# Optimization experiments

Hardware: AMD Instinct MI355X
Metric: run time of the kernel (lower is better)

## Reference

```python
import jax, jax.numpy as jnp
import numpy as np

N = 200000   # nodes
R = 4        # relations
E = 1000000  # edges per relation
B = 1024     # graphs in batch


def _graph_conv(h, s, d, ew, W, b):
    """DGL GraphConv, norm='both', optional edge_weight. h:[N,F_in] -> [N,F_out]."""
    n = h.shape[0]
    ones = jnp.ones(s.shape[0], dtype=h.dtype)
    out_deg = jnp.clip(jax.ops.segment_sum(ones, s, num_segments=n), 1.0)
    in_deg = jnp.clip(jax.ops.segment_sum(ones, d, num_segments=n), 1.0)
    hs = h * jax.lax.rsqrt(out_deg)[:, None]          # src-side norm
    m = hs[s]                                         # gather: [E, F_in]
    if ew is not None:
        m = m * ew[:, None]
    agg = jax.ops.segment_sum(m, d, num_segments=n)   # scatter-sum: [N, F_in]
    rst = agg * jax.lax.rsqrt(in_deg)[:, None]        # dst-side norm
    return rst @ W + b


def _hetero_layer(h, src, dst, ew, W, b):
    out = None
    for r in range(R):
        ewr = None if ew is None else ew[r]
        o = _graph_conv(h, src[r], dst[r], ewr, W[r], b[r])
        out = o if out is None else out + o
    return out


def setup_inputs() -> dict:
    key = jax.random.key(0)
    ks = jax.random.split(key, 10)
    feat = jax.random.normal(ks[0], (N, 2), dtype=jnp.float32)
    src = jax.random.randint(ks[1], (R, E), 0, N, dtype=jnp.int32)
    dst = jax.random.randint(ks[2], (R, E), 0, N, dtype=jnp.int32)
    ew = jax.random.uniform(ks[3], (R, E), dtype=jnp.float32)
    graph_ids = jnp.sort(jax.random.randint(ks[4], (N,), 0, B, dtype=jnp.int32))
    W1 = jax.random.normal(ks[5], (R, 2, 16), dtype=jnp.float32) * 0.5
    b1 = jnp.zeros((R, 16), dtype=jnp.float32)
    W2 = jax.random.normal(ks[6], (R, 16, 16), dtype=jnp.float32) * 0.25
    b2 = jnp.zeros((R, 16), dtype=jnp.float32)
    Wc = jax.random.normal(ks[7], (16, 2), dtype=jnp.float32) * 0.25
    bc = jnp.zeros((2,), dtype=jnp.float32)
    return {"feat": feat, "src": src, "dst": dst, "ew": ew,
            "graph_ids": graph_ids, "W1": W1, "b1": b1,
            "W2": W2, "b2": b2, "Wc": Wc, "bc": bc}


def reference(feat, src, dst, ew, graph_ids, W1, b1, W2, b2, Wc, bc):
    # layer 1: per-relation weighted GraphConv, summed over relations
    h = _hetero_layer(feat, src, dst, ew, W1, b1)
    h = jax.nn.relu(h)
    # layer 2: no edge weights (kwargs not forwarded in original code)
    h = _hetero_layer(h, src, dst, None, W2, b2)
    # mean_nodes per graph in the batch
    sums = jax.ops.segment_sum(h, graph_ids, num_segments=B)          # [B,16]
    cnts = jax.ops.segment_sum(jnp.ones((N,), h.dtype), graph_ids, num_segments=B)
    hg = sums / jnp.clip(cnts, 1.0)[:, None]
    return hg @ Wc + bc                                               # [B,2]
```

## Files before the change

kernel.cpp:

```cpp
#include <hip/hip_runtime.h>
#include <hip/hip_fp16.h>

#define NN 200000
#define RR 4
#define EE 1000000
#define BB 1024
#define RN (RR*NN)

#define BSH 7
#define BSZ 128
#define NB 1563
#define RK (RR*NB)
#define CSH 10
#define CNODES 1024
#define CC 196
#define EPB 16384
#define SBT 1024
#define BPR ((EE + EPB - 1) / EPB)
#define GSLOTS 32
#define STG 6144

#define SRC_OF(u)  (((u) >> 7) & 0x3FFFF)
#define DL_OF(u)   ((int)((u) & 127))
#define DEG_OF(u)  ((u) >> 25)

#define OFF_POOL    0
#define OFF_CNT     (OFF_POOL + BB*16)
#define OFF_CNTS    (OFF_CNT + BB)
#define OFF_CNTD    (OFF_CNTS + RR*CC)
#define OFF_CURS    (OFF_CNTD + RR*CC)
#define OFF_CURD    (OFF_CURS + RR*CC)
#define OFF_GSB     (OFF_CURD + RR*CC)
#define OFF_GDB     (OFF_GSB + RR*CC + 1)
#define OFF_GFIN    (OFF_GDB + RR*CC + 1)
#define OFF_PBCS    (OFF_GFIN + RK + 1)
#define OFF_PBCD    (OFF_PBCS + BPR*RR*CC)
#define ZERO_UNITS_ (OFF_PBCD + BPR*RR*CC)
#define ZERO_UNITS  (ZERO_UNITS_ + (ZERO_UNITS_ & 1))
#define OFF_DEGB    ZERO_UNITS
#define OFF_INVI    (OFF_DEGB + RN/4)
#define OFF_RW16    (OFF_INVI + RN)
#define OFF_AGG1    (OFF_RW16 + RN/2)
#define OFF_SBC     OFF_AGG1
#define OFF_H1H     (OFF_AGG1 + RN*2)
#define OFF_KWC_    (OFF_H1H + NN*8)
#define OFF_KWC     (OFF_KWC_ + (OFF_KWC_ & 1))
#define OFF_KW4     (OFF_KWC + RR*EE*2)


__global__ __launch_bounds__(1024) void k_cnt(const int* __restrict__ src,
                                              const int* __restrict__ dst,
                                              int* __restrict__ cntS,
                                              int* __restrict__ cntD,
                                              int* __restrict__ pbcS,
                                              int* __restrict__ pbcD) {
  __shared__ int hS[CC], hD[CC];
  int t = threadIdx.x, r = blockIdx.y, c0 = blockIdx.x * EPB;
  if (t < CC) { hS[t] = 0; hD[t] = 0; }
  __syncthreads();
  const int4* s4p = (const int4*)(src + (size_t)r * EE + c0);
  const int4* d4p = (const int4*)(dst + (size_t)r * EE + c0);
  int nv = min(EPB, EE - c0) >> 2;
  for (int i = t; i < nv; i += 1024) {
    int4 s = s4p[i], d = d4p[i];
    atomicAdd(&hS[s.x >> CSH], 1); atomicAdd(&hS[s.y >> CSH], 1);
    atomicAdd(&hS[s.z >> CSH], 1); atomicAdd(&hS[s.w >> CSH], 1);
    atomicAdd(&hD[d.x >> CSH], 1); atomicAdd(&hD[d.y >> CSH], 1);
    atomicAdd(&hD[d.z >> CSH], 1); atomicAdd(&hD[d.w >> CSH], 1);
  }
  __syncthreads();
  if (t < CC) {
    size_t pb = (size_t)(blockIdx.x * RR + r) * CC + t;
    pbcS[pb] = hS[t];
    pbcD[pb] = hD[t];
    if (hS[t]) atomicAdd(&cntS[r * CC + t], hS[t]);
    if (hD[t]) atomicAdd(&cntD[r * CC + t], hD[t]);
  }
}

__global__ __launch_bounds__(1024) void k_scan(const int* __restrict__ cntS,
                                               const int* __restrict__ cntD,
                                               int* __restrict__ gsb,
                                               int* __restrict__ gdb,
                                               int* __restrict__ gfin) {
  __shared__ int s[1024];
  int t = threadIdx.x;
  int v = (t < RR * CC) ? cntS[t] : 0;
  s[t] = v;
  __syncthreads();
  for (int off = 1; off < 1024; off <<= 1) {
    int u = (t >= off) ? s[t - off] : 0;
    __syncthreads();
    s[t] += u;
    __syncthreads();
  }
  if (t < RR * CC) {
    int r = t / CC;
    int pre = (r == 0) ? 0 : s[r * CC - 1];
    gsb[t] = r * EE + (s[t] - v) - pre;
  }
  if (t == 0) gsb[RR * CC] = RR * EE;
  __syncthreads();
  int w = (t < RR * CC) ? cntD[t] : 0;
  s[t] = w;
  __syncthreads();
  for (int off = 1; off < 1024; off <<= 1) {
    int u = (t >= off) ? s[t - off] : 0;
    __syncthreads();
    s[t] += u;
    __syncthreads();
  }
  if (t < RR * CC) {
    int r = t / CC;
    int pre = (r == 0) ? 0 : s[r * CC - 1];
    gdb[t] = r * EE + (s[t] - w) - pre;
  }
  if (t == 0) { gdb[RR * CC] = RR * EE; gfin[RK] = RR * EE; }
}

__global__ __launch_bounds__(SBT) void k_part(const int* __restrict__ src,
                                              const int* __restrict__ dst,
                                              const float* __restrict__ ew,
                                              const int* __restrict__ gsb,
                                              const int* __restrict__ gdb,
                                              const int* __restrict__ pbcS,
                                              const int* __restrict__ pbcD,
                                              int* __restrict__ curS,
                                              int* __restrict__ curD,
                                              unsigned short* __restrict__ sbc,
                                              unsigned long long* __restrict__ kwc) {
  __shared__ int bS[CC], lS[CC];
  __shared__ int bD[CC], lD[CC];
  int t = threadIdx.x, r = blockIdx.y, c0 = blockIdx.x * EPB;
  if (t < CC) {
    size_t pb = (size_t)(blockIdx.x * RR + r) * CC + t;
    int kc = r * CC + t;
    int v = pbcS[pb];
    bS[t] = v ? gsb[kc] + atomicAdd(&curS[kc], v) : 0;
    lS[t] = 0;
    int w = pbcD[pb];
    bD[t] = w ? gdb[kc] + atomicAdd(&curD[kc], w) : 0;
    lD[t] = 0;
  }
  __syncthreads();
  const int4*   s4p = (const int4*)  (src + (size_t)r * EE + c0);
  const int4*   d4p = (const int4*)  (dst + (size_t)r * EE + c0);
  const float4* e4p = (const float4*)(ew  + (size_t)r * EE + c0);
  int nv = min(EPB, EE - c0) >> 2;
  for (int i = t; i < nv; i += SBT) {
    int4 s4 = s4p[i], d4 = d4p[i];
    float4 w4 = e4p[i];
    int ss[4] = {s4.x, s4.y, s4.z, s4.w};
    int dd[4] = {d4.x, d4.y, d4.z, d4.w};
    float we[4] = {w4.x, w4.y, w4.z, w4.w};
#pragma unroll
    for (int j = 0; j < 4; j++) {
      int s = ss[j], d = dd[j];
      int cs = s >> CSH;
      sbc[(size_t)bS[cs] + atomicAdd(&lS[cs], 1)] = (unsigned short)(s & (CNODES - 1));
      int cd = d >> CSH;
      unsigned low = (unsigned)(d & (CNODES - 1)) | ((unsigned)s << CSH);
      unsigned long long rec =
          ((unsigned long long)__half_as_ushort(__float2half_rn(we[j])) << 32) | low;
      kwc[(size_t)bD[cd] + atomicAdd(&lD[cd], 1)] = rec;
    }
  }
}

__global__ __launch_bounds__(1024) void k_fineS(const unsigned short* __restrict__ sbc,
                                                const int* __restrict__ gsb,
                                                unsigned char* __restrict__ degb) {
  __shared__ int h[CNODES];
  int t = threadIdx.x, c = blockIdx.x, r = blockIdx.y;
  int kc = r * CC + c;
  int s0 = gsb[kc];
  int m = gsb[kc + 1] - s0;
  h[t] = 0;
  __syncthreads();
  int head = (s0 & 1) && (m > 0) ? 1 : 0;
  if (head && t == 0) atomicAdd(&h[sbc[s0]], 1);
  int mv = (m - head) >> 1;
  const unsigned* p = (const unsigned*)(sbc + s0 + head);
  for (int i = t; i < mv; i += 1024) {
    unsigned v = p[i];
    atomicAdd(&h[v & 0xFFFF], 1);
    atomicAdd(&h[v >> 16], 1);
  }
  if (((m - head) & 1) && t == 1023) atomicAdd(&h[sbc[(size_t)s0 + m - 1]], 1);
  __syncthreads();
  int n = c * CNODES + t;
  if (n < NN) degb[r * NN + n] = (unsigned char)min(max(h[t], 1), 63);
}

__global__ __launch_bounds__(1024) void k_fineD(const unsigned long long* __restrict__ kwc,
                                                const int* __restrict__ gdb,
                                                const unsigned char* __restrict__ degb,
                                                const float* __restrict__ feat,
                                                unsigned* __restrict__ kw4,
                                                int* __restrict__ gfin,
                                                float* __restrict__ invi,
                                                unsigned short* __restrict__ rw16,
                                                float* __restrict__ agg1) {
  __shared__ unsigned long long buf[STG];
  __shared__ int h[CNODES];
  __shared__ float la[CNODES * 2];
  __shared__ int s4[1024];
  __shared__ int sfb[8];
  int t = threadIdx.x, c = blockIdx.x, r = blockIdx.y;
  int kc = r * CC + c;
  int b0 = gdb[kc];
  int nrec = gdb[kc + 1] - b0;
  int stg = min(nrec, STG);
  h[t] = 0; la[t] = 0.f; la[t + CNODES] = 0.f;
  for (int i = t; i < stg; i += 1024) buf[i] = kwc[(size_t)b0 + i];
  __syncthreads();
  for (int i = t; i < nrec; i += 1024) {
    unsigned low = (unsigned)((i < STG) ? buf[i] : kwc[(size_t)b0 + i]);
    atomicAdd(&h[low & (CNODES - 1)], 1);
  }
  __syncthreads();
  int cntt = h[t];
  s4[t] = cntt;
  __syncthreads();
  for (int off = 1; off < 1024; off <<= 1) {
    int v = (t >= off) ? s4[t - off] : 0;
    __syncthreads();
    s4[t] += v;
    __syncthreads();
  }
  int base = s4[t] - cntt;
  if ((t & 127) == 0) sfb[t >> 7] = base;
  __syncthreads();
  int n0 = c * CNODES;
  {
    int n = n0 + t;
    if (n < NN) {
      invi[r * NN + n] = rsqrtf((float)max(cntt, 1));
      rw16[r * NN + n] = (unsigned short)(base - sfb[t >> 7]);
    }
  }
  if (t < 8) {
    int kb = c * 8 + t;
    if (kb < NB) gfin[r * NB + kb] = b0 + sfb[t];
  }
  __syncthreads();
  h[t] = base;
  __syncthreads();
  for (int i = t; i < nrec; i += 1024) {
    unsigned long long rc = (i < STG) ? buf[i] : kwc[(size_t)b0 + i];
    unsigned low = (unsigned)rc;
    int dcl = low & (CNODES - 1);
    int s = low >> CSH;
    float ewf = __half2float(__ushort_as_half((unsigned short)(rc >> 32)));
    unsigned dg = degb[r * NN + s];
    float w1 = ewf * rsqrtf((float)dg);
    float2 fv = ((const float2*)feat)[s];
    atomicAdd(&la[dcl * 2],     fv.x * w1);
    atomicAdd(&la[dcl * 2 + 1], fv.y * w1);
    int pos = atomicAdd(&h[dcl], 1);
    kw4[(size_t)b0 + pos] = ((unsigned)dcl & 127u) | ((unsigned)s << 7) | (dg << 25);
  }
  __syncthreads();
  {
    int n = n0 + t;
    if (n < NN)
      ((float2*)agg1)[r * NN + n] = make_float2(la[t * 2], la[t * 2 + 1]);
  }
}

__device__ __forceinline__ unsigned pack2h(float a, float b) {
  __half2 h = __floats2half2_rn(a, b);
  return *reinterpret_cast<unsigned*>(&h);
}

__global__ __launch_bounds__(256) void k_l1b(const float* __restrict__ agg1,
                                             const float* __restrict__ invi,
                                             const float* __restrict__ W1,
                                             const float* __restrict__ b1,
                                             __half* __restrict__ h1h) {
  __shared__ float sW[RR * 2 * 16];
  __shared__ float sb[16];
  int t = threadIdx.x, b = blockIdx.x;
  if (t < RR * 2 * 16) sW[t] = W1[t];
  if (t < 16) {
    float s = 0.f;
    for (int r = 0; r < RR; r++) s += b1[r * 16 + t];
    sb[t] = s;
  }
  __syncthreads();
  int n = b * 256 + t;
  if (n >= NN) return;
  float acc[16];
#pragma unroll
  for (int j = 0; j < 16; j++) acc[j] = sb[j];
#pragma unroll
  for (int r = 0; r < RR; r++) {
    float iv = invi[r * NN + n];
    float2 a = ((const float2*)agg1)[r * NN + n];
    float a0 = a.x * iv, a1 = a.y * iv;
#pragma unroll
    for (int j = 0; j < 16; j++)
      acc[j] += a0 * sW[(r * 2 + 0) * 16 + j] + a1 * sW[(r * 2 + 1) * 16 + j];
  }
#pragma unroll
  for (int j = 0; j < 16; j++) acc[j] = fmaxf(acc[j], 0.f);
  uint4 u0, u1;
  u0.x = pack2h(acc[0], acc[1]);  u0.y = pack2h(acc[2], acc[3]);
  u0.z = pack2h(acc[4], acc[5]);  u0.w = pack2h(acc[6], acc[7]);
  u1.x = pack2h(acc[8], acc[9]);  u1.y = pack2h(acc[10], acc[11]);
  u1.z = pack2h(acc[12], acc[13]); u1.w = pack2h(acc[14], acc[15]);
  uint4* o = (uint4*)(h1h + (size_t)n * 16);
  o[0] = u0; o[1] = u1;
}

__device__ __forceinline__ void acc8(float* acc, uint4 u, float w) {
  float2 p;
  p = __half22float2(*(__half2*)&u.x); acc[0] += p.x * w; acc[1] += p.y * w;
  p = __half22float2(*(__half2*)&u.y); acc[2] += p.x * w; acc[3] += p.y * w;
  p = __half22float2(*(__half2*)&u.z); acc[4] += p.x * w; acc[5] += p.y * w;
  p = __half22float2(*(__half2*)&u.w); acc[6] += p.x * w; acc[7] += p.y * w;
}

__global__ __launch_bounds__(256) void k_l2(const unsigned* __restrict__ kw4,
                                            const int* __restrict__ gfin,
                                            const unsigned short* __restrict__ rw16,
                                            const __half* __restrict__ h1h,
                                            const float* __restrict__ invi,
                                            const float* __restrict__ W2,
                                            const int* __restrict__ gid,
                                            float* __restrict__ pool,
                                            float* __restrict__ cnt) {
  __shared__ float agg[BSZ * 17];
  __shared__ float sW4[RR * 256];
  __shared__ int   sg[BSZ];
  __shared__ unsigned short srw[BSZ + 2];
  __shared__ float gslot[GSLOTS * 16];
  __shared__ int   cslot[GSLOTS];
  __shared__ int   present[GSLOTS];
  int t = threadIdx.x, b = blockIdx.x;
  int n0 = b << BSH;
#pragma unroll
  for (int r = 0; r < RR; r++) sW4[r * 256 + t] = W2[r * 256 + t];
  if (t < GSLOTS) { cslot[t] = 0; present[t] = 0; }
  for (int i = t; i < GSLOTS * 16; i += 256) gslot[i] = 0.f;
  int n = n0 + t;
  bool valid = (t < BSZ) && (n < NN);
  float out[16];
#pragma unroll
  for (int j = 0; j < 16; j++) out[j] = 0.f;
  const uint4* h4p = (const uint4*)h1h;
  int f8 = t & 1, g = t >> 1;

  for (int r = 0; r < RR; r++) {
    int k = r * NB + b;
    int base = gfin[k];
    int m = gfin[k + 1] - base;
    __syncthreads();
    if (t < BSZ) {
      int nn_ = n0 + t;
      srw[t] = (nn_ < NN) ? rw16[r * NN + nn_] : (unsigned short)m;
    }
    if (t == BSZ) srw[BSZ] = (unsigned short)m;
    __syncthreads();
    const unsigned* rb = kw4 + (size_t)base;
    int e = srw[g], en = srw[g + 1];
    float acc[8];
#pragma unroll
    for (int j = 0; j < 8; j++) acc[j] = 0.f;
    for (; e + 3 < en; e += 4) {
      unsigned r0 = rb[e], r1 = rb[e + 1], r2 = rb[e + 2], r3 = rb[e + 3];
      uint4 u0 = h4p[(size_t)SRC_OF(r0) * 2 + f8];
      uint4 u1 = h4p[(size_t)SRC_OF(r1) * 2 + f8];
      uint4 u2 = h4p[(size_t)SRC_OF(r2) * 2 + f8];
      uint4 u3 = h4p[(size_t)SRC_OF(r3) * 2 + f8];
      acc8(acc, u0, rsqrtf((float)DEG_OF(r0)));
      acc8(acc, u1, rsqrtf((float)DEG_OF(r1)));
      acc8(acc, u2, rsqrtf((float)DEG_OF(r2)));
      acc8(acc, u3, rsqrtf((float)DEG_OF(r3)));
    }
    for (; e < en; e++) {
      unsigned rr = rb[e];
      uint4 u = h4p[(size_t)SRC_OF(rr) * 2 + f8];
      acc8(acc, u, rsqrtf((float)DEG_OF(rr)));
    }
#pragma unroll
    for (int j = 0; j < 8; j++) agg[g * 17 + 8 * f8 + j] = acc[j];
    __syncthreads();
    if (valid) {
      float iv = invi[r * NN + n];
#pragma unroll
      for (int kk = 0; kk < 16; kk++) {
        float a = agg[t * 17 + kk] * iv;
#pragma unroll
        for (int j = 0; j < 16; j++) out[j] += a * sW4[r * 256 + kk * 16 + j];
      }
    }
  }
  __syncthreads();
  int g0 = gid[n0];
  if (t < BSZ) {
    sg[t] = valid ? (gid[n] - g0) : -1;
#pragma unroll
    for (int j = 0; j < 16; j++) agg[t * 17 + j] = out[j];
  }
  __syncthreads();
  {
    int f = t & 15, i0 = t >> 4;
    for (int i = i0; i < BSZ; i += 16) {
      int gsN = sg[i];
      if (gsN < 0) continue;
      float v = agg[i * 17 + f];
      if (gsN < GSLOTS) {
        atomicAdd(&gslot[gsN * 16 + f], v);
        if (f == 0) {
          present[gsN] = 1;
          atomicAdd(&cslot[gsN], 1);
        }
      } else {
        atomicAdd(&pool[(g0 + gsN) * 16 + f], v);
        if (f == 0) atomicAdd(&cnt[g0 + gsN], 1.0f);
      }
    }
  }
  __syncthreads();
  if (t < GSLOTS * 16) {
    int gsN = t >> 4, f = t & 15;
    if (present[gsN]) atomicAdd(&pool[(g0 + gsN) * 16 + f], gslot[t]);
  }
  if (t < GSLOTS && cslot[t] > 0)
    atomicAdd(&cnt[g0 + t], (float)cslot[t]);
}

__global__ __launch_bounds__(256) void k_final(const float* __restrict__ pool,
                                               const float* __restrict__ cnt,
                                               const float* __restrict__ b2,
                                               const float* __restrict__ Wc,
                                               const float* __restrict__ bc,
                                               float* __restrict__ out) {
  int b = blockIdx.x * 256 + threadIdx.x;
  if (b >= BB) return;
  float c = cnt[b];
  float inv = 1.0f / fmaxf(c, 1.0f);
  float o0 = bc[0], o1 = bc[1];
#pragma unroll
  for (int j = 0; j < 16; j++) {
    float sb = 0.f;
    for (int r = 0; r < RR; r++) sb += b2[r * 16 + j];
    float v = (pool[b * 16 + j] + c * sb) * inv;
    o0 += v * Wc[j * 2 + 0];
    o1 += v * Wc[j * 2 + 1];
  }
  out[b * 2 + 0] = o0;
  out[b * 2 + 1] = o1;
}

extern "C" void kernel_launch(void* const* d_in, const int* in_sizes, int n_in,
                              void* d_out, int out_size, void* d_ws, size_t ws_size,
                              hipStream_t stream) {
  const float* feat = (const float*)d_in[0];
  const int*   src  = (const int*)d_in[1];
  const int*   dst  = (const int*)d_in[2];
  const float* ew   = (const float*)d_in[3];
  const int*   gid  = (const int*)d_in[4];
  const float* W1   = (const float*)d_in[5];
  const float* b1   = (const float*)d_in[6];
  const float* W2   = (const float*)d_in[7];
  const float* b2   = (const float*)d_in[8];
  const float* Wc   = (const float*)d_in[9];
  const float* bc   = (const float*)d_in[10];

  char* ws = (char*)d_ws;
  float* pool   = (float*)(ws + (size_t)OFF_POOL * 4);
  float* cnt    = (float*)(ws + (size_t)OFF_CNT  * 4);
  int*   cntS   = (int*)  (ws + (size_t)OFF_CNTS * 4);
  int*   cntD   = (int*)  (ws + (size_t)OFF_CNTD * 4);
  int*   curS   = (int*)  (ws + (size_t)OFF_CURS * 4);
  int*   curD   = (int*)  (ws + (size_t)OFF_CURD * 4);
  int*   gsb    = (int*)  (ws + (size_t)OFF_GSB  * 4);
  int*   gdb    = (int*)  (ws + (size_t)OFF_GDB  * 4);
  int*   gfin   = (int*)  (ws + (size_t)OFF_GFIN * 4);
  int*   pbcS   = (int*)  (ws + (size_t)OFF_PBCS * 4);
  int*   pbcD   = (int*)  (ws + (size_t)OFF_PBCD * 4);
  unsigned char*  degb = (unsigned char*) (ws + (size_t)OFF_DEGB * 4);
  float* invi   = (float*)(ws + (size_t)OFF_INVI * 4);
  unsigned short* rw16 = (unsigned short*)(ws + (size_t)OFF_RW16 * 4);
  float* agg1   = (float*)(ws + (size_t)OFF_AGG1 * 4);
  unsigned short* sbc  = (unsigned short*)(ws + (size_t)OFF_SBC * 4);
  __half* h1h   = (__half*)(ws + (size_t)OFF_H1H * 4);
  unsigned long long* kwc = (unsigned long long*)(ws + (size_t)OFF_KWC * 4);
  unsigned* kw4 = (unsigned*)(ws + (size_t)OFF_KW4 * 4);

  hipMemsetAsync(d_ws, 0, (size_t)ZERO_UNITS * 4, stream);

  k_cnt   <<<dim3(BPR, RR), 1024, 0, stream>>>(src, dst, cntS, cntD, pbcS, pbcD);
  k_scan  <<<1, 1024, 0, stream>>>(cntS, cntD, gsb, gdb, gfin);
  k_part  <<<dim3(BPR, RR), SBT, 0, stream>>>(src, dst, ew, gsb, gdb, pbcS, pbcD,
                                              curS, curD, sbc, kwc);
  k_fineS <<<dim3(CC, RR), 1024, 0, stream>>>(sbc, gsb, degb);
  k_fineD <<<dim3(CC, RR), 1024, 0, stream>>>(kwc, gdb, degb, feat, kw4, gfin, invi, rw16, agg1);
  k_l1b   <<<(NN + 255) / 256, 256, 0, stream>>>(agg1, invi, W1, b1, h1h);
  k_l2    <<<NB, 256, 0, stream>>>(kw4, gfin, rw16, h1h, invi, W2, gid, pool, cnt);
  k_final <<<(BB + 255) / 256, 256, 0, stream>>>(pool, cnt, b2, Wc, bc, (float*)d_out);
}
```

Measured before the change: 305.9 us.

## Stage partitioned edges in LDS and write buckets out contiguously

Result: slower. 317.3 us (+3.7%).

```diff
diff --git a/kernel.cpp b/kernel.cpp
--- a/kernel.cpp
+++ b/kernel.cpp
@@ -14,7 +14,7 @@
 #define CSH 10
 #define CNODES 1024
 #define CC 196
-#define EPB 16384
+#define EPB 4096
 #define SBT 1024
 #define BPR ((EE + EPB - 1) / EPB)
 #define GSLOTS 32
@@ -129,41 +129,79 @@
                                               int* __restrict__ curD,
                                               unsigned short* __restrict__ sbc,
                                               unsigned long long* __restrict__ kwc) {
-  __shared__ int bS[CC], lS[CC];
-  __shared__ int bD[CC], lD[CC];
+  __shared__ unsigned long long rbuf[EPB];
+  __shared__ unsigned short sbuf[EPB];
+  __shared__ int s4[1024];
+  __shared__ int ofS[CC + 1], ofD[CC + 1];
+  __shared__ int bS[CC], bD[CC];
+  __shared__ int lS[CC], lD[CC];
   int t = threadIdx.x, r = blockIdx.y, c0 = blockIdx.x * EPB;
+  int ne = min(EPB, EE - c0);
+  int vS = 0, vD = 0;
   if (t < CC) {
     size_t pb = (size_t)(blockIdx.x * RR + r) * CC + t;
     int kc = r * CC + t;
-    int v = pbcS[pb];
-    bS[t] = v ? gsb[kc] + atomicAdd(&curS[kc], v) : 0;
-    lS[t] = 0;
-    int w = pbcD[pb];
-    bD[t] = w ? gdb[kc] + atomicAdd(&curD[kc], w) : 0;
-    lD[t] = 0;
-  }
+    vS = pbcS[pb];
+    vD = pbcD[pb];
+    bS[t] = vS ? gsb[kc] + atomicAdd(&curS[kc], vS) : 0;
+    bD[t] = vD ? gdb[kc] + atomicAdd(&curD[kc], vD) : 0;
+    lS[t] = 0; lD[t] = 0;
+  }
+  s4[t] = (t < CC) ? vS : 0;
+  __syncthreads();
+  for (int off = 1; off < 1024; off <<= 1) {
+    int u = (t >= off) ? s4[t - off] : 0;
+    __syncthreads();
+    s4[t] += u;
+    __syncthreads();
+  }
+  if (t < CC) ofS[t] = s4[t] - vS;
+  if (t == 0) ofS[CC] = ne;
+  __syncthreads();
+  s4[t] = (t < CC) ? vD : 0;
+  __syncthreads();
+  for (int off = 1; off < 1024; off <<= 1) {
+    int u = (t >= off) ? s4[t - off] : 0;
+    __syncthreads();
+    s4[t] += u;
+    __syncthreads();
+  }
+  if (t < CC) ofD[t] = s4[t] - vD;
+  if (t == 0) ofD[CC] = ne;
   __syncthreads();
   const int4*   s4p = (const int4*)  (src + (size_t)r * EE + c0);
   const int4*   d4p = (const int4*)  (dst + (size_t)r * EE + c0);
   const float4* e4p = (const float4*)(ew  + (size_t)r * EE + c0);
-  int nv = min(EPB, EE - c0) >> 2;
+  int nv = ne >> 2;
   for (int i = t; i < nv; i += SBT) {
-    int4 s4 = s4p[i], d4 = d4p[i];
-    float4 w4 = e4p[i];
-    int ss[4] = {s4.x, s4.y, s4.z, s4.w};
-    int dd[4] = {d4.x, d4.y, d4.z, d4.w};
-    float we[4] = {w4.x, w4.y, w4.z, w4.w};
+    int4 sv = s4p[i], dv = d4p[i];
+    float4 wv = e4p[i];
+    int ss[4] = {sv.x, sv.y, sv.z, sv.w};
+    int dd[4] = {dv.x, dv.y, dv.z, dv.w};
+    float we[4] = {wv.x, wv.y, wv.z, wv.w};
 #pragma unroll
     for (int j = 0; j < 4; j++) {
       int s = ss[j], d = dd[j];
       int cs = s >> CSH;
-      sbc[(size_t)bS[cs] + atomicAdd(&lS[cs], 1)] = (unsigned short)(s & (CNODES - 1));
+      int ps = atomicAdd(&lS[cs], 1);
+      sbuf[ofS[cs] + ps] = (unsigned short)(s & (CNODES - 1));
       int cd = d >> CSH;
+      int pd = atomicAdd(&lD[cd], 1);
       unsigned low = (unsigned)(d & (CNODES - 1)) | ((unsigned)s << CSH);
-      unsigned long long rec =
+      rbuf[ofD[cd] + pd] =
           ((unsigned long long)__half_as_ushort(__float2half_rn(we[j])) << 32) | low;
-      kwc[(size_t)bD[cd] + atomicAdd(&lD[cd], 1)] = rec;
-    }
+    }
+  }
+  __syncthreads();
+  for (int i = t; i < ne; i += SBT) {
+    int lo = 0, hi = CC;
+    while (hi - lo > 1) { int mid = (lo + hi) >> 1; if (ofD[mid] <= i) lo = mid; else hi = mid; }
+    kwc[(size_t)bD[lo] + (i - ofD[lo])] = rbuf[i];
+  }
+  for (int i = t; i < ne; i += SBT) {
+    int lo = 0, hi = CC;
+    while (hi - lo > 1) { int mid = (lo + hi) >> 1; if (ofS[mid] <= i) lo = mid; else hi = mid; }
+    sbc[(size_t)bS[lo] + (i - ofS[lo])] = sbuf[i];
   }
 }
 
```
